# Performance work log

Hardware: AMD Instinct MI355X
Metric: run time of the kernel (lower is better)

Reference implementation:

```python
import jax, jax.numpy as jnp
import numpy as np

NUM_CLASSES = 200
MARGIN = 0.6
LAMBDA_WEIGHT = 0.2
ALPHA = 1.5
GAMMA = 0.8
EPS = 1e-8


def setup_inputs() -> dict:
    key = jax.random.key(0)
    k1, k2 = jax.random.split(key)
    B, D = 32768, 512
    features = jax.random.normal(k1, (B, D), dtype=jnp.float32)
    labels = jax.random.randint(k2, (B,), 0, NUM_CLASSES, dtype=jnp.int64)
    return {"features": features, "labels": labels}


def reference(features, labels):
    B, D = features.shape
    C = NUM_CLASSES
    labels = labels.astype(jnp.int32)

    # Per-class prototypes (segment mean), matching mask-sum / (count + eps)
    proto_sum = jax.ops.segment_sum(features, labels, num_segments=C)      # [C, D]
    counts = jax.ops.segment_sum(jnp.ones((B,), features.dtype), labels, num_segments=C)
    prototypes = proto_sum / (counts[:, None] + EPS)                       # [C, D]

    # Squared distances from every sample to every prototype via Gram trick
    f2 = jnp.sum(features * features, axis=1, keepdims=True)               # [B, 1]
    p2 = jnp.sum(prototypes * prototypes, axis=1)                          # [C]
    d2 = jnp.maximum(f2 + p2[None, :] - 2.0 * features @ prototypes.T, 0.0)  # [B, C]

    # Nearest negative prototype: mask out the positive class with +inf
    pos_mask = jnp.arange(C)[None, :] == labels[:, None]                   # [B, C]
    neg_idx = jnp.argmin(jnp.where(pos_mask, jnp.inf, d2), axis=1)         # [B]

    # Exact squared distances to positive / chosen negative prototypes
    pos_proto = prototypes[labels]                                         # [B, D]
    neg_proto = prototypes[neg_idx]                                        # [B, D]
    d_ap = jnp.sum((features - pos_proto) ** 2, axis=1)                    # [B]
    d_an = jnp.sum((features - neg_proto) ** 2, axis=1)                    # [B]

    # Replicate the original's sequential normalization (d_ap is updated first)
    d_ap_n = d_ap / (d_ap + d_an + EPS)
    d_an_n = d_an / (d_ap_n + d_an + EPS)

    per_sample = jnp.maximum(0.0, ALPHA * d_ap_n - GAMMA * d_an_n + MARGIN)
    contrastive_loss = jnp.mean(per_sample)
    return jnp.abs(LAMBDA_WEIGHT * contrastive_loss)
```

## Files before the change

kernel.cpp:

```cpp
#include <hip/hip_runtime.h>
#include <hip/hip_bf16.h>

#define NCLS 200
#define NPADP 224
#define NROWS 256
#define NTW 7
#define DIM 512
#define NSAMP 32768
#define NSEG 8
#define CAP 32
#define BM 64
#define BK 32
#define KIT 16
#define CHUS (NROWS*32)

typedef __attribute__((ext_vector_type(4))) float f32x4;
typedef __attribute__((ext_vector_type(4))) int   i32x4;
typedef __attribute__((ext_vector_type(8))) short bf16x8;

__device__ inline short bf16s(float x) {
  __hip_bfloat16 h = __float2bfloat16(x);
  return *reinterpret_cast<short*>(&h);
}

__device__ inline bf16x8 pack8(f32x4 a, f32x4 b) {
  bf16x8 r;
  r[0] = bf16s(a[0]); r[1] = bf16s(a[1]); r[2] = bf16s(a[2]); r[3] = bf16s(a[3]);
  r[4] = bf16s(b[0]); r[5] = bf16s(b[1]); r[6] = bf16s(b[2]); r[7] = bf16s(b[3]);
  return r;
}

__device__ inline float sumsq(f32x4 a) {
  return a[0]*a[0] + a[1]*a[1] + a[2]*a[2] + a[3]*a[3];
}

__global__ __launch_bounds__(512) void k_psum(
    const float* __restrict__ feat, const int* __restrict__ labels,
    float* __restrict__ psum, int* __restrict__ pcnt)
{
  const int bx = blockIdx.x;
  const int c = bx >> 3, s = bx & 7;
  const int tid = threadIdx.x;
  const int lane = tid & 63;
  const int w = tid >> 6;

  __shared__ int   lists[8][CAP];
  __shared__ int   cnts[8];
  __shared__ float partial[8][DIM];

  int cnt = 0;
  const int segbase = s * (NSAMP / NSEG) + w * (NSAMP / NSEG / 8);
  #pragma unroll
  for (int i = 0; i < 2; ++i) {
    const int base = segbase + i * 256 + lane * 4;
    const i32x4 lab4 = *(const i32x4*)(labels + base);
    #pragma unroll
    for (int u = 0; u < 4; ++u) {
      const bool m = (lab4[u] == c);
      const unsigned long long bal = __ballot(m);
      if (m) {
        const int pos = cnt + __popcll(bal & ((1ull << lane) - 1ull));
        if (pos < CAP) lists[w][pos] = base + u;
      }
      cnt += __popcll(bal);
    }
  }
  if (cnt > CAP) cnt = CAP;
  if (lane == 0) cnts[w] = cnt;

  float aE[8], aO[8];
  #pragma unroll
  for (int q = 0; q < 8; ++q) { aE[q] = 0.f; aO[q] = 0.f; }
  int j = 0;
  for (; j + 2 <= cnt; j += 2) {
    const int r0 = lists[w][j], r1 = lists[w][j + 1];
    const f32x4 a0 = *(const f32x4*)(feat + (size_t)r0 * DIM + lane * 8);
    const f32x4 b0 = *(const f32x4*)(feat + (size_t)r0 * DIM + lane * 8 + 4);
    const f32x4 a1 = *(const f32x4*)(feat + (size_t)r1 * DIM + lane * 8);
    const f32x4 b1 = *(const f32x4*)(feat + (size_t)r1 * DIM + lane * 8 + 4);
    aE[0] += a0[0]; aE[1] += a0[1]; aE[2] += a0[2]; aE[3] += a0[3];
    aE[4] += b0[0]; aE[5] += b0[1]; aE[6] += b0[2]; aE[7] += b0[3];
    aO[0] += a1[0]; aO[1] += a1[1]; aO[2] += a1[2]; aO[3] += a1[3];
    aO[4] += b1[0]; aO[5] += b1[1]; aO[6] += b1[2]; aO[7] += b1[3];
  }
  if (j < cnt) {
    const int r0 = lists[w][j];
    const f32x4 a0 = *(const f32x4*)(feat + (size_t)r0 * DIM + lane * 8);
    const f32x4 b0 = *(const f32x4*)(feat + (size_t)r0 * DIM + lane * 8 + 4);
    aE[0] += a0[0]; aE[1] += a0[1]; aE[2] += a0[2]; aE[3] += a0[3];
    aE[4] += b0[0]; aE[5] += b0[1]; aE[6] += b0[2]; aE[7] += b0[3];
  }
  #pragma unroll
  for (int q = 0; q < 8; ++q) partial[w][lane * 8 + q] = aE[q] + aO[q];
  __syncthreads();

  int total = 0;
  #pragma unroll
  for (int u = 0; u < 8; ++u) total += cnts[u];
  float sv = 0.f;
  #pragma unroll
  for (int u = 0; u < 8; ++u) sv += partial[u][tid];
  psum[(size_t)(s * NCLS + c) * DIM + tid] = sv;
  if (tid == 0) pcnt[s * NCLS + c] = total;
}

__global__ __launch_bounds__(256) void k_pcomb(
    const float* __restrict__ psum, const int* __restrict__ pcnt,
    unsigned short* __restrict__ protoI, float* __restrict__ p2out)
{
  const int c = blockIdx.x;
  const int tid = threadIdx.x;
  const int sw = (c >> 1) & 3;
  if (c >= NCLS) {
    #pragma unroll
    for (int h = 0; h < 2; ++h) {
      const int d = tid + h * 256;
      const int ck = d >> 5, uL = (d >> 3) & 3, e = d & 7;
      protoI[(size_t)ck * CHUS + c * 32 + (uL ^ sw) * 8 + e] = 0;
    }
    if (tid == 0) p2out[c] = 1e30f;
    return;
  }
  __shared__ float red[256];
  float a0 = 0.f, a1 = 0.f;
  int total = 0;
  #pragma unroll
  for (int s = 0; s < NSEG; ++s) {
    a0 += psum[(size_t)(s * NCLS + c) * DIM + tid];
    a1 += psum[(size_t)(s * NCLS + c) * DIM + 256 + tid];
    total += pcnt[s * NCLS + c];
  }
  const float inv = 1.0f / ((float)total + 1e-8f);
  const float p0 = a0 * inv, p1 = a1 * inv;
  {
    const int d = tid;
    const int ck = d >> 5, uL = (d >> 3) & 3, e = d & 7;
    protoI[(size_t)ck * CHUS + c * 32 + (uL ^ sw) * 8 + e] = (unsigned short)bf16s(p0);
  }
  {
    const int d = tid + 256;
    const int ck = d >> 5, uL = (d >> 3) & 3, e = d & 7;
    protoI[(size_t)ck * CHUS + c * 32 + (uL ^ sw) * 8 + e] = (unsigned short)bf16s(p1);
  }

  red[tid] = p0 * p0 + p1 * p1;
  __syncthreads();
  for (int st = 128; st > 0; st >>= 1) {
    if (tid < st) red[tid] += red[tid + st];
    __syncthreads();
  }
  if (tid == 0) p2out[c] = red[0];
}

__global__ __launch_bounds__(256) void k_score(
    const float* __restrict__ feat, const int* __restrict__ labels,
    const unsigned short* __restrict__ protoI, const float* __restrict__ p2,
    float* __restrict__ partials)
{
  __shared__ __align__(16) unsigned short As[2][BM * BK];
  __shared__ __align__(1024) unsigned short Bs[2][CHUS];
  __shared__ float f2s[BM][4];
  __shared__ float rd_d[2][BM];
  __shared__ int   rd_c[2][BM];
  __shared__ float rd_p[2][BM];

  const int tid = threadIdx.x;
  const int lane = tid & 63;
  const int w = tid >> 6;
  const int wm = w >> 1, wn = w & 1;
  const int lr = lane & 15;
  const int kg = lane >> 4;
  const int blockRow = blockIdx.x * BM;

  const int arow = tid >> 2, apart = tid & 3;
  const float* agp = feat + (size_t)(blockRow + arow) * DIM + apart * 8;
  const int aoff = arow * BK + ((apart ^ (arow & 3)) * 8);

  float f2part = 0.f;

  f32x4 acc0[NTW], acc1[NTW];
  #pragma unroll
  for (int n = 0; n < NTW; ++n) {
    acc0[n] = f32x4{0.f, 0.f, 0.f, 0.f};
    acc1[n] = f32x4{0.f, 0.f, 0.f, 0.f};
  }

  const int r0v = wm * 32 + lr;
  const int r1v = r0v + 16;
  const int ar0 = r0v * BK + ((kg ^ (r0v & 3)) * 8);
  const int ar1 = r1v * BK + ((kg ^ (r1v & 3)) * 8);

#define ISSUE_A(T, S) do {                                                      \
    const float* ag_ = agp + (T) * BK;                                          \
    S##0 = *(const f32x4*)(ag_);                                                \
    S##1 = *(const f32x4*)(ag_ + 4);                                            \
  } while (0)

#define STOREA(NB, S) do {                                                      \
    f2part += sumsq(S##0) + sumsq(S##1);                                        \
    *(bf16x8*)&As[NB][aoff] = pack8(S##0, S##1);                                \
  } while (0)

#define BGLD(T, NB) do {                                                        \
    _Pragma("unroll")                                                           \
    for (int i_ = 0; i_ < 4; ++i_) {                                            \
      const int j_ = w * 4 + i_;                                                \
      const unsigned short* g_ = protoI + (size_t)(T) * CHUS + j_ * 512 + lane * 8; \
      unsigned short* l_ = &Bs[NB][j_ * 512];                                   \
      __builtin_amdgcn_global_load_lds(                                         \
          (const __attribute__((address_space(1))) void*)g_,                    \
          (__attribute__((address_space(3))) void*)l_, 16, 0, 0);               \
    }                                                                           \
  } while (0)

#define COMPUTE(CUR) do {                                                       \
    const bf16x8 Af0 = *(const bf16x8*)&As[CUR][ar0];                           \
    const bf16x8 Af1 = *(const bf16x8*)&As[CUR][ar1];                           \
    _Pragma("unroll")                                                           \
    for (int n = 0; n < NTW; ++n) {                                             \
      const int row_ = wn * 112 + n * 16 + lr;                                  \
      const bf16x8 Bf = *(const bf16x8*)&Bs[CUR][row_ * 32 + ((kg ^ ((row_ >> 1) & 3)) * 8)]; \
      acc0[n] = __builtin_amdgcn_mfma_f32_16x16x32_bf16(Af0, Bf, acc0[n], 0, 0, 0); \
      acc1[n] = __builtin_amdgcn_mfma_f32_16x16x32_bf16(Af1, Bf, acc1[n], 0, 0, 0); \
    }                                                                           \
  } while (0)

#define BAR_VM2() do {                                                          \
    asm volatile("s_waitcnt vmcnt(2)" ::: "memory");                            \
    asm volatile("s_waitcnt lgkmcnt(0)" ::: "memory");                          \
    __builtin_amdgcn_s_barrier();                                               \
  } while (0)

#define BAR_VM0() do {                                                          \
    asm volatile("s_waitcnt vmcnt(0)" ::: "memory");                            \
    asm volatile("s_waitcnt lgkmcnt(0)" ::: "memory");                          \
    __builtin_amdgcn_s_barrier();                                               \
  } while (0)

  f32x4 AE_0, AE_1;
  f32x4 AO_0, AO_1;

  ISSUE_A(0, AE_);
  BGLD(0, 0);
  __builtin_amdgcn_sched_barrier(0);
  ISSUE_A(1, AO_);
  STOREA(0, AE_);
  BAR_VM2();

  #pragma unroll
  for (int t = 0; t < KIT; ++t) {
    const int cur = t & 1;
    const int nxt = cur ^ 1;
    if (t + 1 < KIT) {
      if ((t & 1) == 0) STOREA(nxt, AO_); else STOREA(nxt, AE_);
      BGLD(t + 1, nxt);
      __builtin_amdgcn_sched_barrier(0);
    }
    if (t + 2 < KIT) {
      if ((t & 1) == 0) ISSUE_A(t + 2, AE_); else ISSUE_A(t + 2, AO_);
    }
    COMPUTE(cur);
    if (t + 1 < KIT) {
      if (t + 2 < KIT) BAR_VM2(); else BAR_VM0();
    }
  }
#undef ISSUE_A
#undef STOREA
#undef BGLD
#undef COMPUTE
#undef BAR_VM2
#undef BAR_VM0

  f2s[arow][apart] = f2part;
  __syncthreads();

  float p2v[NTW];
  #pragma unroll
  for (int n = 0; n < NTW; ++n) p2v[n] = p2[wn * 112 + n * 16 + lr];

  #pragma unroll
  for (int m = 0; m < 2; ++m) {
    #pragma unroll
    for (int r = 0; r < 4; ++r) {
      const int srow = kg * 4 + r;
      const int lrow = wm * 32 + m * 16 + srow;
      const float f2v = (f2s[lrow][0] + f2s[lrow][1]) + (f2s[lrow][2] + f2s[lrow][3]);
      const int lab = labels[blockRow + lrow];
      float bestd = 1e38f; int bestc = 1 << 30;
      float posd = -1.f;
      #pragma unroll
      for (int n = 0; n < NTW; ++n) {
        const int cidx = wn * 112 + n * 16 + lr;
        const float sc = (m == 0) ? acc0[n][r] : acc1[n][r];
        const float d2 = fmaxf(f2v + p2v[n] - 2.0f * sc, 0.0f);
        if (cidx == lab) posd = d2;
        else if (cidx < NCLS &&
                 (d2 < bestd || (d2 == bestd && cidx < bestc))) { bestd = d2; bestc = cidx; }
      }
      #pragma unroll
      for (int sft = 1; sft < 16; sft <<= 1) {
        const float od = __shfl_xor(bestd, sft);
        const int   oc = __shfl_xor(bestc, sft);
        const float op = __shfl_xor(posd, sft);
        if (od < bestd || (od == bestd && oc < bestc)) { bestd = od; bestc = oc; }
        posd = fmaxf(posd, op);
      }
      if (lr == 0) {
        rd_d[wn][lrow] = bestd; rd_c[wn][lrow] = bestc; rd_p[wn][lrow] = posd;
      }
    }
  }
  __syncthreads();

  if (tid < BM) {
    const float d0 = rd_d[0][tid], d1 = rd_d[1][tid];
    const int   c0 = rd_c[0][tid], c1 = rd_c[1][tid];
    float bestd;
    if (d1 < d0 || (d1 == d0 && c1 < c0)) bestd = d1;
    else                                  bestd = d0;
    const float posd = fmaxf(rd_p[0][tid], rd_p[1][tid]);
    const float dap = posd, dan = bestd;
    const float dapn = dap / (dap + dan + 1e-8f);
    const float dann = dan / (dapn + dan + 1e-8f);
    float v = fmaxf(0.f, 1.5f * dapn - 0.8f * dann + 0.6f);
    #pragma unroll
    for (int sft = 1; sft < 64; sft <<= 1) v += __shfl_xor(v, sft);
    if (tid == 0) partials[blockIdx.x] = v;
  }
}

__global__ __launch_bounds__(256) void k_finish(const float* __restrict__ partials,
                                                float* __restrict__ out)
{
  __shared__ float red[256];
  const int tid = threadIdx.x;
  red[tid] = partials[tid] + partials[tid + 256];
  __syncthreads();
  for (int st = 128; st > 0; st >>= 1) {
    if (tid < st) red[tid] += red[tid + st];
    __syncthreads();
  }
  if (tid == 0) out[0] = fabsf(0.2f * (red[0] / (float)NSAMP));
}

extern "C" void kernel_launch(void* const* d_in, const int* in_sizes, int n_in,
                              void* d_out, int out_size, void* d_ws, size_t ws_size,
                              hipStream_t stream) {
  const float* feat = (const float*)d_in[0];
  const int* labels = (const int*)d_in[1];
  float* out = (float*)d_out;

  char* ws = (char*)d_ws;
  unsigned short* protoI = (unsigned short*)ws;
  float* p2 = (float*)(ws + 262144);
  float* partials = (float*)(ws + 263168);
  float* psum = (float*)(ws + 266240);
  int* pcnt = (int*)(ws + 266240 + 3276800);

  k_psum<<<NSEG * NCLS, 512, 0, stream>>>(feat, labels, psum, pcnt);
  k_pcomb<<<NPADP, 256, 0, stream>>>(psum, pcnt, protoI, p2);
  k_score<<<512, 256, 0, stream>>>(feat, labels, protoI, p2, partials);
  k_finish<<<1, 256, 0, stream>>>(partials, out);
}
```

Baseline: 46.09 us.

## Fuse prototype combine and final reduction into producer kernels via atomic tickets

Merges the prototype-combine kernel into the partial-sum kernel: the last 224 blocks to finish, identified by an atomic ticket counter, spin until every block has arrived and then each builds one prototype row and its squared norm. The final loss reduction is likewise folded into the score kernel, where the last block to finish sums the per-block partials. This removes two kernel launches and their gaps but adds a memset, atomics, spin-waiting and fences. The spin-wait is deadlock-free only because those blocks are the last to take tickets.

```diff
diff --git a/kernel.cpp b/kernel.cpp
--- a/kernel.cpp
+++ b/kernel.cpp
@@ -13,6 +13,8 @@
 #define BK 32
 #define KIT 16
 #define CHUS (NROWS*32)
+#define NB1 (NSEG*NCLS)
+#define NB2 512
 
 typedef __attribute__((ext_vector_type(4))) float f32x4;
 typedef __attribute__((ext_vector_type(4))) int   i32x4;
@@ -34,9 +36,11 @@
   return a[0]*a[0] + a[1]*a[1] + a[2]*a[2] + a[3]*a[3];
 }
 
-__global__ __launch_bounds__(512) void k_psum(
+__global__ __launch_bounds__(512) void k_proto(
     const float* __restrict__ feat, const int* __restrict__ labels,
-    float* __restrict__ psum, int* __restrict__ pcnt)
+    float* __restrict__ psum, int* __restrict__ pcnt,
+    unsigned short* __restrict__ protoI, float* __restrict__ p2out,
+    unsigned int* __restrict__ cnt1)
 {
   const int bx = blockIdx.x;
   const int c = bx >> 3, s = bx & 7;
@@ -47,6 +51,7 @@
   __shared__ int   lists[8][CAP];
   __shared__ int   cnts[8];
   __shared__ float partial[8][DIM];
+  __shared__ unsigned int tsh;
 
   int cnt = 0;
   const int segbase = s * (NSAMP / NSEG) + w * (NSAMP / NSEG / 8);
@@ -102,60 +107,56 @@
   for (int u = 0; u < 8; ++u) sv += partial[u][tid];
   psum[(size_t)(s * NCLS + c) * DIM + tid] = sv;
   if (tid == 0) pcnt[s * NCLS + c] = total;
-}
-
-__global__ __launch_bounds__(256) void k_pcomb(
-    const float* __restrict__ psum, const int* __restrict__ pcnt,
-    unsigned short* __restrict__ protoI, float* __restrict__ p2out)
-{
-  const int c = blockIdx.x;
-  const int tid = threadIdx.x;
-  const int sw = (c >> 1) & 3;
-  if (c >= NCLS) {
-    #pragma unroll
-    for (int h = 0; h < 2; ++h) {
-      const int d = tid + h * 256;
-      const int ck = d >> 5, uL = (d >> 3) & 3, e = d & 7;
-      protoI[(size_t)ck * CHUS + c * 32 + (uL ^ sw) * 8 + e] = 0;
-    }
-    if (tid == 0) p2out[c] = 1e30f;
+
+  __syncthreads();
+  if (tid == 0) {
+    __threadfence();
+    tsh = atomicAdd(cnt1, 1u);
+  }
+  __syncthreads();
+  const unsigned int ticket = tsh;
+  if (ticket < (unsigned)(NB1 - NPADP)) return;
+  const int cc = (int)(ticket - (unsigned)(NB1 - NPADP));
+
+  if (tid == 0) {
+    while (atomicAdd(cnt1, 0u) < (unsigned)NB1) __builtin_amdgcn_s_sleep(8);
+  }
+  __syncthreads();
+  __threadfence();
+
+  const int sw = (cc >> 1) & 3;
+  const int d = tid;
+  const int ck = d >> 5, uL = (d >> 3) & 3, e = d & 7;
+  if (cc >= NCLS) {
+    protoI[(size_t)ck * CHUS + cc * 32 + (uL ^ sw) * 8 + e] = 0;
+    if (tid == 0) p2out[cc] = 1e30f;
     return;
   }
-  __shared__ float red[256];
-  float a0 = 0.f, a1 = 0.f;
-  int total = 0;
-  #pragma unroll
-  for (int s = 0; s < NSEG; ++s) {
-    a0 += psum[(size_t)(s * NCLS + c) * DIM + tid];
-    a1 += psum[(size_t)(s * NCLS + c) * DIM + 256 + tid];
-    total += pcnt[s * NCLS + c];
-  }
-  const float inv = 1.0f / ((float)total + 1e-8f);
-  const float p0 = a0 * inv, p1 = a1 * inv;
-  {
-    const int d = tid;
-    const int ck = d >> 5, uL = (d >> 3) & 3, e = d & 7;
-    protoI[(size_t)ck * CHUS + c * 32 + (uL ^ sw) * 8 + e] = (unsigned short)bf16s(p0);
-  }
-  {
-    const int d = tid + 256;
-    const int ck = d >> 5, uL = (d >> 3) & 3, e = d & 7;
-    protoI[(size_t)ck * CHUS + c * 32 + (uL ^ sw) * 8 + e] = (unsigned short)bf16s(p1);
-  }
-
-  red[tid] = p0 * p0 + p1 * p1;
-  __syncthreads();
-  for (int st = 128; st > 0; st >>= 1) {
+  float a = 0.f;
+  int tot = 0;
+  #pragma unroll
+  for (int q = 0; q < NSEG; ++q) {
+    a += psum[(size_t)(q * NCLS + cc) * DIM + d];
+    tot += pcnt[q * NCLS + cc];
+  }
+  const float p = a / ((float)tot + 1e-8f);
+  protoI[(size_t)ck * CHUS + cc * 32 + (uL ^ sw) * 8 + e] = (unsigned short)bf16s(p);
+
+  float* red = &partial[0][0];
+  red[tid] = p * p;
+  __syncthreads();
+  for (int st = 256; st > 0; st >>= 1) {
     if (tid < st) red[tid] += red[tid + st];
     __syncthreads();
   }
-  if (tid == 0) p2out[c] = red[0];
+  if (tid == 0) p2out[cc] = red[0];
 }
 
 __global__ __launch_bounds__(256) void k_score(
     const float* __restrict__ feat, const int* __restrict__ labels,
     const unsigned short* __restrict__ protoI, const float* __restrict__ p2,
-    float* __restrict__ partials)
+    float* __restrict__ partials, float* __restrict__ out,
+    unsigned int* __restrict__ cnt2)
 {
   __shared__ __align__(16) unsigned short As[2][BM * BK];
   __shared__ __align__(1024) unsigned short Bs[2][CHUS];
@@ -163,6 +164,7 @@
   __shared__ float rd_d[2][BM];
   __shared__ int   rd_c[2][BM];
   __shared__ float rd_p[2][BM];
+  __shared__ unsigned int tsh;
 
   const int tid = threadIdx.x;
   const int lane = tid & 63;
@@ -327,20 +329,24 @@
     for (int sft = 1; sft < 64; sft <<= 1) v += __shfl_xor(v, sft);
     if (tid == 0) partials[blockIdx.x] = v;
   }
-}
-
-__global__ __launch_bounds__(256) void k_finish(const float* __restrict__ partials,
-                                                float* __restrict__ out)
-{
-  __shared__ float red[256];
-  const int tid = threadIdx.x;
-  red[tid] = partials[tid] + partials[tid + 256];
-  __syncthreads();
-  for (int st = 128; st > 0; st >>= 1) {
-    if (tid < st) red[tid] += red[tid + st];
+
+  __syncthreads();
+  if (tid == 0) {
+    __threadfence();
+    tsh = atomicAdd(cnt2, 1u);
+  }
+  __syncthreads();
+  if (tsh == (unsigned)(NB2 - 1)) {
+    __threadfence();
+    float* red = &f2s[0][0];
+    red[tid] = partials[tid] + partials[tid + 256];
     __syncthreads();
-  }
-  if (tid == 0) out[0] = fabsf(0.2f * (red[0] / (float)NSAMP));
+    for (int st = 128; st > 0; st >>= 1) {
+      if (tid < st) red[tid] += red[tid + st];
+      __syncthreads();
+    }
+    if (tid == 0) out[0] = fabsf(0.2f * (red[0] / (float)NSAMP));
+  }
 }
 
 extern "C" void kernel_launch(void* const* d_in, const int* in_sizes, int n_in,
@@ -354,11 +360,12 @@
   unsigned short* protoI = (unsigned short*)ws;
   float* p2 = (float*)(ws + 262144);
   float* partials = (float*)(ws + 263168);
+  unsigned int* cnt1 = (unsigned int*)(ws + 265216);
+  unsigned int* cnt2 = (unsigned int*)(ws + 265216 + 128);
   float* psum = (float*)(ws + 266240);
   int* pcnt = (int*)(ws + 266240 + 3276800);
 
-  k_psum<<<NSEG * NCLS, 512, 0, stream>>>(feat, labels, psum, pcnt);
-  k_pcomb<<<NPADP, 256, 0, stream>>>(psum, pcnt, protoI, p2);
-  k_score<<<512, 256, 0, stream>>>(feat, labels, protoI, p2, partials);
-  k_finish<<<1, 256, 0, stream>>>(partials, out);
-}
+  hipMemsetAsync(ws + 265216, 0, 256, stream);
+  k_proto<<<NB1, 512, 0, stream>>>(feat, labels, psum, pcnt, protoI, p2, cnt1);
+  k_score<<<NB2, 256, 0, stream>>>(feat, labels, protoI, p2, partials, out, cnt2);
+}
```

After: 159.0 us. 3.45x slower.

## Deepen score-kernel prefetch pipeline to triple-buffered B tiles and three A stages

Applied to the files above, without the earlier changes.

Changes the k_score main loop from double-buffered prototype tiles to triple-buffered LDS tiles, with the prototype loads issued two iterations ahead. Feature loads now rotate through three register stages and are issued three iterations ahead. The vmcnt waits are adjusted so more global loads stay in flight across each barrier, aiming to hide global memory latency. This costs extra LDS for the third B buffer and more registers, which may reduce occupancy.

```diff
diff --git a/kernel.cpp b/kernel.cpp
--- a/kernel.cpp
+++ b/kernel.cpp
@@ -158,7 +158,7 @@
     float* __restrict__ partials)
 {
   __shared__ __align__(16) unsigned short As[2][BM * BK];
-  __shared__ __align__(1024) unsigned short Bs[2][CHUS];
+  __shared__ __align__(1024) unsigned short Bs[3][CHUS];
   __shared__ float f2s[BM][4];
   __shared__ float rd_d[2][BM];
   __shared__ int   rd_c[2][BM];
@@ -213,20 +213,26 @@
     }                                                                           \
   } while (0)
 
-#define COMPUTE(CUR) do {                                                       \
-    const bf16x8 Af0 = *(const bf16x8*)&As[CUR][ar0];                           \
-    const bf16x8 Af1 = *(const bf16x8*)&As[CUR][ar1];                           \
+#define COMPUTE(CURA, CURB) do {                                                \
+    const bf16x8 Af0 = *(const bf16x8*)&As[CURA][ar0];                          \
+    const bf16x8 Af1 = *(const bf16x8*)&As[CURA][ar1];                          \
     _Pragma("unroll")                                                           \
     for (int n = 0; n < NTW; ++n) {                                             \
       const int row_ = wn * 112 + n * 16 + lr;                                  \
-      const bf16x8 Bf = *(const bf16x8*)&Bs[CUR][row_ * 32 + ((kg ^ ((row_ >> 1) & 3)) * 8)]; \
+      const bf16x8 Bf = *(const bf16x8*)&Bs[CURB][row_ * 32 + ((kg ^ ((row_ >> 1) & 3)) * 8)]; \
       acc0[n] = __builtin_amdgcn_mfma_f32_16x16x32_bf16(Af0, Bf, acc0[n], 0, 0, 0); \
       acc1[n] = __builtin_amdgcn_mfma_f32_16x16x32_bf16(Af1, Bf, acc1[n], 0, 0, 0); \
     }                                                                           \
   } while (0)
 
-#define BAR_VM2() do {                                                          \
-    asm volatile("s_waitcnt vmcnt(2)" ::: "memory");                            \
+#define BAR_VM8() do {                                                          \
+    asm volatile("s_waitcnt vmcnt(8)" ::: "memory");                            \
+    asm volatile("s_waitcnt lgkmcnt(0)" ::: "memory");                          \
+    __builtin_amdgcn_s_barrier();                                               \
+  } while (0)
+
+#define BAR_VM6() do {                                                          \
+    asm volatile("s_waitcnt vmcnt(6)" ::: "memory");                            \
     asm volatile("s_waitcnt lgkmcnt(0)" ::: "memory");                          \
     __builtin_amdgcn_s_barrier();                                               \
   } while (0)
@@ -237,38 +243,44 @@
     __builtin_amdgcn_s_barrier();                                               \
   } while (0)
 
-  f32x4 AE_0, AE_1;
-  f32x4 AO_0, AO_1;
-
-  ISSUE_A(0, AE_);
+  f32x4 S0_0, S0_1, S1_0, S1_1, S2_0, S2_1;
+
+  ISSUE_A(0, S0_);
   BGLD(0, 0);
+  BGLD(1, 1);
   __builtin_amdgcn_sched_barrier(0);
-  ISSUE_A(1, AO_);
-  STOREA(0, AE_);
-  BAR_VM2();
+  ISSUE_A(1, S1_);
+  ISSUE_A(2, S2_);
+  STOREA(0, S0_);
+  BAR_VM8();
 
   #pragma unroll
   for (int t = 0; t < KIT; ++t) {
-    const int cur = t & 1;
-    const int nxt = cur ^ 1;
     if (t + 1 < KIT) {
-      if ((t & 1) == 0) STOREA(nxt, AO_); else STOREA(nxt, AE_);
-      BGLD(t + 1, nxt);
-      __builtin_amdgcn_sched_barrier(0);
-    }
-    if (t + 2 < KIT) {
-      if ((t & 1) == 0) ISSUE_A(t + 2, AE_); else ISSUE_A(t + 2, AO_);
-    }
-    COMPUTE(cur);
+      if (((t + 1) % 3) == 0) STOREA((t + 1) & 1, S0_);
+      else if (((t + 1) % 3) == 1) STOREA((t + 1) & 1, S1_);
+      else STOREA((t + 1) & 1, S2_);
+    }
+    if (t + 2 < KIT) BGLD(t + 2, (t + 2) % 3);
+    __builtin_amdgcn_sched_barrier(0);
+    if (t + 3 < KIT) {
+      if ((t % 3) == 0) ISSUE_A(t + 3, S0_);
+      else if ((t % 3) == 1) ISSUE_A(t + 3, S1_);
+      else ISSUE_A(t + 3, S2_);
+    }
+    COMPUTE(t & 1, t % 3);
     if (t + 1 < KIT) {
-      if (t + 2 < KIT) BAR_VM2(); else BAR_VM0();
+      if (t <= KIT - 4) BAR_VM8();
+      else if (t == KIT - 3) BAR_VM6();
+      else BAR_VM0();
     }
   }
 #undef ISSUE_A
 #undef STOREA
 #undef BGLD
 #undef COMPUTE
-#undef BAR_VM2
+#undef BAR_VM8
+#undef BAR_VM6
 #undef BAR_VM0
 
   f2s[arow][apart] = f2part;
```

After: 43.73 us. 5.1% less time.
